# Kernel optimization log

Hardware: AMD Instinct MI355X
Metric: run time of the kernel (lower is better)

## Reference

```python
import jax, jax.numpy as jnp
import numpy as np

B, N, F, H = 1, 8192, 512, 64
NEG_BIAS = -9.0  # GAT adjacency bias for non-edges


def setup_inputs() -> dict:
    key = jax.random.key(0)
    ks = jax.random.split(key, 6)
    features = jax.random.normal(ks[0], (B, N, F), dtype=jnp.float32)
    edge = jax.random.uniform(ks[1], (B, N, N)) < 0.02
    bias_mat = jnp.where(edge, 0.0, NEG_BIAS).astype(jnp.float32)
    W = jax.random.normal(ks[2], (F, H), dtype=jnp.float32) * 0.05   # 1x1 conv, no bias
    a1 = jax.random.normal(ks[3], (H, 1), dtype=jnp.float32) * 0.05  # f_1 1x1 conv
    b1 = jnp.zeros((1,), dtype=jnp.float32)
    a2 = jax.random.normal(ks[4], (H, 1), dtype=jnp.float32) * 0.05  # f_2 1x1 conv
    b2 = jnp.zeros((1,), dtype=jnp.float32)
    return {"features": features, "bias_mat": bias_mat, "W": W,
            "a1": a1, "b1": b1, "a2": a2, "b2": b2}


def reference(features, bias_mat, W, a1, b1, a2, b2):
    # 1x1 conv projection (no bias): [B,N,F] @ [F,H] -> [B,N,H]
    fts = jnp.einsum('bnf,fh->bnh', features, W)
    # per-node scalar attention terms: [B,N,1]
    f1 = jnp.einsum('bnh,ho->bno', fts, a1) + b1
    f2 = jnp.einsum('bnh,ho->bno', fts, a2) + b2
    # additive pairwise logits: [B,N,N]
    logits = f1 + jnp.swapaxes(f2, 1, 2)
    # masked softmax over neighbors, then (as written in source) add bias again
    coefs = jax.nn.softmax(jax.nn.relu(logits) + bias_mat, axis=-1) + bias_mat
    # weighted aggregation: [B,N,N] @ [B,N,H] -> [B,N,H]
    vals = jnp.einsum('bmn,bnh->bmh', coefs, fts)
    return jax.nn.elu(vals)
```

## Files before the change

kernel.cpp:

```cpp
#include <hip/hip_runtime.h>
#include <math.h>

#define N 8192
#define FDIM 512
#define H 64
#define SEG 192

typedef float vf4 __attribute__((ext_vector_type(4)));

__global__ __launch_bounds__(256) void k_fts(const float* __restrict__ feat,
                                             const float* __restrict__ W,
                                             const float* __restrict__ a1v,
                                             const float* __restrict__ b1v,
                                             const float* __restrict__ a2v,
                                             const float* __restrict__ b2v,
                                             float* __restrict__ fts,
                                             float* __restrict__ f1,
                                             float* __restrict__ f2,
                                             float* __restrict__ T) {
    __shared__ float At[64][34];
    __shared__ float Bf[64][64];
    __shared__ float colred[16][64];
    const int t = threadIdx.x;
    const int row0 = blockIdx.x * 32;
    const int hq = (t & 15) * 4;
    const int rq = (t >> 4) * 2;
    float acc[2][4] = {};
    for (int k0 = 0; k0 < FDIM; k0 += 64) {
#pragma unroll
        for (int i = 0; i < 2; ++i) {
            int l = t + i * 256;
            int r = l >> 4;
            int c4 = (l & 15) * 4;
            float4 av = *(const float4*)&feat[(size_t)(row0 + r) * FDIM + k0 + c4];
            At[c4 + 0][r] = av.x; At[c4 + 1][r] = av.y;
            At[c4 + 2][r] = av.z; At[c4 + 3][r] = av.w;
        }
#pragma unroll
        for (int i = 0; i < 4; ++i) {
            int l = t + i * 256;
            int r = l >> 4;
            int c4 = (l & 15) * 4;
            *(float4*)&Bf[r][c4] = *(const float4*)&W[(size_t)(k0 + r) * H + c4];
        }
        __syncthreads();
#pragma unroll 8
        for (int kk = 0; kk < 64; ++kk) {
            float2 a = *(const float2*)&At[kk][rq];
            float4 b = *(const float4*)&Bf[kk][hq];
            acc[0][0] += a.x * b.x; acc[0][1] += a.x * b.y;
            acc[0][2] += a.x * b.z; acc[0][3] += a.x * b.w;
            acc[1][0] += a.y * b.x; acc[1][1] += a.y * b.y;
            acc[1][2] += a.y * b.z; acc[1][3] += a.y * b.w;
        }
        __syncthreads();
    }
#pragma unroll
    for (int j = 0; j < 2; ++j) {
        float4 v = make_float4(acc[j][0], acc[j][1], acc[j][2], acc[j][3]);
        *(float4*)&fts[(size_t)(row0 + rq + j) * H + hq] = v;
    }
    float pa1[4], pa2[4];
#pragma unroll
    for (int i = 0; i < 4; ++i) { pa1[i] = a1v[hq + i]; pa2[i] = a2v[hq + i]; }
#pragma unroll
    for (int j = 0; j < 2; ++j) {
        float s1 = acc[j][0] * pa1[0] + acc[j][1] * pa1[1] + acc[j][2] * pa1[2] + acc[j][3] * pa1[3];
        float s2 = acc[j][0] * pa2[0] + acc[j][1] * pa2[1] + acc[j][2] * pa2[2] + acc[j][3] * pa2[3];
#pragma unroll
        for (int o = 8; o; o >>= 1) { s1 += __shfl_xor(s1, o); s2 += __shfl_xor(s2, o); }
        if ((t & 15) == 0) {
            f1[row0 + rq + j] = s1 + b1v[0];
            f2[row0 + rq + j] = s2 + b2v[0];
        }
    }
#pragma unroll
    for (int i = 0; i < 4; ++i)
        colred[t >> 4][hq + i] = acc[0][i] + acc[1][i];
    __syncthreads();
    if (t < H) {
        float s = 0.f;
#pragma unroll
        for (int g = 0; g < 16; ++g) s += colred[g][t];
        atomicAdd(&T[t], s);
    }
}

__global__ __launch_bounds__(256) void k_all(const float* __restrict__ bias,
                                             const float* __restrict__ fts,
                                             const float* __restrict__ f1g,
                                             const float* __restrict__ f2g,
                                             const float* __restrict__ T,
                                             float* __restrict__ out) {
    __shared__ int    list[4 * SEG];
    __shared__ float2 pairBuf[4 * SEG];
    __shared__ float  redW[4][64];
    __shared__ float  redF[4][64];
    __shared__ float  redE[4];
    const int t = threadIdx.x;
    const int lane = t & 63;
    const int w = t >> 6;
    const int m = blockIdx.x;
    const float f1m = f1g[m];

    const vf4* p = (const vf4*)(bias + (size_t)m * N) + w * 512 + lane;
    vf4 r[8];
#pragma unroll
    for (int j = 0; j < 8; ++j) r[j] = __builtin_nontemporal_load(&p[j * 64]);
    int c = 0;
#pragma unroll
    for (int j = 0; j < 8; ++j)
        c += (r[j].x == 0.f) + (r[j].y == 0.f) + (r[j].z == 0.f) + (r[j].w == 0.f);
    int sc = c;
#pragma unroll
    for (int o = 1; o < 64; o <<= 1) {
        int u = __shfl_up(sc, o);
        if (lane >= o) sc += u;
    }
    const int segBase = w * SEG;
    int pos = segBase + sc - c;
#pragma unroll
    for (int j = 0; j < 8; ++j) {
        int nb = (w * 512 + j * 64 + lane) * 4;
        int m0 = (r[j].x == 0.f), m1 = (r[j].y == 0.f);
        int m2 = (r[j].z == 0.f), m3 = (r[j].w == 0.f);
        if (m0) list[pos] = nb;
        int p1 = pos + m0;
        if (m1) list[p1] = nb + 1;
        int p2 = p1 + m1;
        if (m2) list[p2] = nb + 2;
        int p3 = p2 + m2;
        if (m3) list[p3] = nb + 3;
        pos = p3 + m3;
    }
    int cw = __shfl(sc, 63);
    cw = __builtin_amdgcn_readfirstlane(cw);
    if (cw > SEG) cw = SEG;

    for (int l = lane; l < cw; l += 64) {
        int n = list[segBase + l];
        float ff = f2g[n];
        float ee = __expf(fmaxf(f1m + ff, 0.f));
        pairBuf[segBase + l] = make_float2(ee, __int_as_float(n * 256));
    }

    const char* ftsB = (const char*)fts;
    const int laneOff = lane * 4;
    float accW = 0.f, accF = 0.f, accE = 0.f;
    for (int e = 0; e < cw; e += 8) {
        float2 pr[8];
#pragma unroll
        for (int j = 0; j < 8; ++j) {
            int idx = (e + j < cw) ? (e + j) : (cw - 1);
            pr[j] = pairBuf[segBase + idx];
        }
        float vv[8];
#pragma unroll
        for (int j = 0; j < 8; ++j)
            vv[j] = *(const float*)(ftsB + __float_as_int(pr[j].y) + laneOff);
#pragma unroll
        for (int j = 0; j < 8; ++j) {
            if (e + j < cw) {
                accW += pr[j].x * vv[j];
                accF += vv[j];
                accE += pr[j].x;
            }
        }
    }
    redW[w][lane] = accW;
    redF[w][lane] = accF;
    if (lane == 0) redE[w] = accE;
    __syncthreads();

    if (t < H) {
        float eW = redW[0][t] + redW[1][t] + redW[2][t] + redW[3][t];
        float eF = redF[0][t] + redF[1][t] + redF[2][t] + redF[3][t];
        float eE = redE[0] + redE[1] + redE[2] + redE[3];
        float S = (eE > 0.f) ? eW / eE : 0.f;
        float val = S - 9.0f * (T[t] - eF);
        out[(size_t)m * H + t] = val > 0.f ? val : expm1f(val);
    }
}

extern "C" void kernel_launch(void* const* d_in, const int* in_sizes, int n_in,
                              void* d_out, int out_size, void* d_ws, size_t ws_size,
                              hipStream_t stream) {
    const float* feat = (const float*)d_in[0];
    const float* bias = (const float*)d_in[1];
    const float* W    = (const float*)d_in[2];
    const float* a1   = (const float*)d_in[3];
    const float* b1   = (const float*)d_in[4];
    const float* a2   = (const float*)d_in[5];
    const float* b2   = (const float*)d_in[6];
    float* out = (float*)d_out;

    float* ws  = (float*)d_ws;
    float* fts = ws;
    float* f1  = fts + (size_t)N * H;
    float* f2  = f1 + N;
    float* T   = f2 + N;

    (void)hipMemsetAsync(T, 0, H * sizeof(float), stream);
    hipLaunchKernelGGL(k_fts, dim3(N / 32), dim3(256), 0, stream,
                       feat, W, a1, b1, a2, b2, fts, f1, f2, T);
    hipLaunchKernelGGL(k_all, dim3(N), dim3(256), 0, stream,
                       bias, fts, f1, f2, T, out);
}
```

Before: 390.8 us.

## Use ballot-based compaction, padded edge lists, and smaller projection tiles

Replaces the per-lane count plus shfl_up scan in edge-list compaction with a ballot/mbcnt per element, which removes the scan. The edge list is padded to a multiple of 8 with zero-weight entries that point at a zeroed scratch row, so the gather loop runs without per-element bounds checks and reads pairBuf as float4. The projection kernel now uses 16-row tiles, doubling its block count, and k_all gains an occupancy hint. Costs: more ballots and LDS writes, plus a larger memset to zero the scratch row.

```diff
diff --git a/kernel.cpp b/kernel.cpp
--- a/kernel.cpp
+++ b/kernel.cpp
@@ -5,6 +5,7 @@
 #define FDIM 512
 #define H 64
 #define SEG 192
+#define ZOFF ((N * H + 2 * N + H) * 4)
 
 typedef float vf4 __attribute__((ext_vector_type(4)));
 
@@ -18,65 +19,53 @@
                                              float* __restrict__ f1,
                                              float* __restrict__ f2,
                                              float* __restrict__ T) {
-    __shared__ float At[64][34];
+    __shared__ float At[64][17];
     __shared__ float Bf[64][64];
     __shared__ float colred[16][64];
     const int t = threadIdx.x;
-    const int row0 = blockIdx.x * 32;
+    const int row0 = blockIdx.x * 16;
     const int hq = (t & 15) * 4;
-    const int rq = (t >> 4) * 2;
-    float acc[2][4] = {};
+    const int rq = t >> 4;
+    float acc[4] = {};
     for (int k0 = 0; k0 < FDIM; k0 += 64) {
-#pragma unroll
-        for (int i = 0; i < 2; ++i) {
-            int l = t + i * 256;
-            int r = l >> 4;
-            int c4 = (l & 15) * 4;
+        {
+            const int r = t >> 4;
+            const int c4 = (t & 15) * 4;
             float4 av = *(const float4*)&feat[(size_t)(row0 + r) * FDIM + k0 + c4];
             At[c4 + 0][r] = av.x; At[c4 + 1][r] = av.y;
             At[c4 + 2][r] = av.z; At[c4 + 3][r] = av.w;
         }
 #pragma unroll
         for (int i = 0; i < 4; ++i) {
-            int l = t + i * 256;
-            int r = l >> 4;
-            int c4 = (l & 15) * 4;
-            *(float4*)&Bf[r][c4] = *(const float4*)&W[(size_t)(k0 + r) * H + c4];
+            const int l = t + i * 256;
+            const int rr = l >> 4;
+            const int c4 = (l & 15) * 4;
+            *(float4*)&Bf[rr][c4] = *(const float4*)&W[(size_t)(k0 + rr) * H + c4];
         }
         __syncthreads();
 #pragma unroll 8
         for (int kk = 0; kk < 64; ++kk) {
-            float2 a = *(const float2*)&At[kk][rq];
-            float4 b = *(const float4*)&Bf[kk][hq];
-            acc[0][0] += a.x * b.x; acc[0][1] += a.x * b.y;
-            acc[0][2] += a.x * b.z; acc[0][3] += a.x * b.w;
-            acc[1][0] += a.y * b.x; acc[1][1] += a.y * b.y;
-            acc[1][2] += a.y * b.z; acc[1][3] += a.y * b.w;
+            const float a = At[kk][rq];
+            const float4 b = *(const float4*)&Bf[kk][hq];
+            acc[0] += a * b.x; acc[1] += a * b.y;
+            acc[2] += a * b.z; acc[3] += a * b.w;
         }
         __syncthreads();
     }
-#pragma unroll
-    for (int j = 0; j < 2; ++j) {
-        float4 v = make_float4(acc[j][0], acc[j][1], acc[j][2], acc[j][3]);
-        *(float4*)&fts[(size_t)(row0 + rq + j) * H + hq] = v;
-    }
+    *(float4*)&fts[(size_t)(row0 + rq) * H + hq] = make_float4(acc[0], acc[1], acc[2], acc[3]);
     float pa1[4], pa2[4];
 #pragma unroll
     for (int i = 0; i < 4; ++i) { pa1[i] = a1v[hq + i]; pa2[i] = a2v[hq + i]; }
+    float s1 = acc[0] * pa1[0] + acc[1] * pa1[1] + acc[2] * pa1[2] + acc[3] * pa1[3];
+    float s2 = acc[0] * pa2[0] + acc[1] * pa2[1] + acc[2] * pa2[2] + acc[3] * pa2[3];
 #pragma unroll
-    for (int j = 0; j < 2; ++j) {
-        float s1 = acc[j][0] * pa1[0] + acc[j][1] * pa1[1] + acc[j][2] * pa1[2] + acc[j][3] * pa1[3];
-        float s2 = acc[j][0] * pa2[0] + acc[j][1] * pa2[1] + acc[j][2] * pa2[2] + acc[j][3] * pa2[3];
-#pragma unroll
-        for (int o = 8; o; o >>= 1) { s1 += __shfl_xor(s1, o); s2 += __shfl_xor(s2, o); }
-        if ((t & 15) == 0) {
-            f1[row0 + rq + j] = s1 + b1v[0];
-            f2[row0 + rq + j] = s2 + b2v[0];
-        }
+    for (int o = 8; o; o >>= 1) { s1 += __shfl_xor(s1, o); s2 += __shfl_xor(s2, o); }
+    if ((t & 15) == 0) {
+        f1[row0 + rq] = s1 + b1v[0];
+        f2[row0 + rq] = s2 + b2v[0];
     }
 #pragma unroll
-    for (int i = 0; i < 4; ++i)
-        colred[t >> 4][hq + i] = acc[0][i] + acc[1][i];
+    for (int i = 0; i < 4; ++i) colred[rq][hq + i] = acc[i];
     __syncthreads();
     if (t < H) {
         float s = 0.f;
@@ -86,14 +75,14 @@
     }
 }
 
-__global__ __launch_bounds__(256) void k_all(const float* __restrict__ bias,
-                                             const float* __restrict__ fts,
-                                             const float* __restrict__ f1g,
-                                             const float* __restrict__ f2g,
-                                             const float* __restrict__ T,
-                                             float* __restrict__ out) {
+__global__ __launch_bounds__(256, 4) void k_all(const float* __restrict__ bias,
+                                                const float* __restrict__ fts,
+                                                const float* __restrict__ f1g,
+                                                const float* __restrict__ f2g,
+                                                const float* __restrict__ T,
+                                                float* __restrict__ out) {
     __shared__ int    list[4 * SEG];
-    __shared__ float2 pairBuf[4 * SEG];
+    __shared__ __align__(16) float2 pairBuf[4 * SEG];
     __shared__ float  redW[4][64];
     __shared__ float  redF[4][64];
     __shared__ float  redE[4];
@@ -107,64 +96,57 @@
     vf4 r[8];
 #pragma unroll
     for (int j = 0; j < 8; ++j) r[j] = __builtin_nontemporal_load(&p[j * 64]);
-    int c = 0;
-#pragma unroll
-    for (int j = 0; j < 8; ++j)
-        c += (r[j].x == 0.f) + (r[j].y == 0.f) + (r[j].z == 0.f) + (r[j].w == 0.f);
-    int sc = c;
-#pragma unroll
-    for (int o = 1; o < 64; o <<= 1) {
-        int u = __shfl_up(sc, o);
-        if (lane >= o) sc += u;
-    }
+
     const int segBase = w * SEG;
-    int pos = segBase + sc - c;
+    int base = segBase;
 #pragma unroll
     for (int j = 0; j < 8; ++j) {
-        int nb = (w * 512 + j * 64 + lane) * 4;
-        int m0 = (r[j].x == 0.f), m1 = (r[j].y == 0.f);
-        int m2 = (r[j].z == 0.f), m3 = (r[j].w == 0.f);
-        if (m0) list[pos] = nb;
-        int p1 = pos + m0;
-        if (m1) list[p1] = nb + 1;
-        int p2 = p1 + m1;
-        if (m2) list[p2] = nb + 2;
-        int p3 = p2 + m2;
-        if (m3) list[p3] = nb + 3;
-        pos = p3 + m3;
+        const int nb = (w * 512 + j * 64 + lane) * 4;
+#pragma unroll
+        for (int k = 0; k < 4; ++k) {
+            const float v = (k == 0) ? r[j].x : (k == 1) ? r[j].y : (k == 2) ? r[j].z : r[j].w;
+            const bool e = (v == 0.f);
+            const unsigned long long mk = __ballot(e);
+            const int below = __builtin_amdgcn_mbcnt_hi((unsigned)(mk >> 32),
+                              __builtin_amdgcn_mbcnt_lo((unsigned)mk, 0));
+            if (e) list[base + below] = nb + k;
+            base += (int)__popcll(mk);
+        }
     }
-    int cw = __shfl(sc, 63);
-    cw = __builtin_amdgcn_readfirstlane(cw);
+    int cw = base - segBase;
     if (cw > SEG) cw = SEG;
+    const int cwPad = (cw + 7) & ~7;
 
-    for (int l = lane; l < cw; l += 64) {
-        int n = list[segBase + l];
-        float ff = f2g[n];
-        float ee = __expf(fmaxf(f1m + ff, 0.f));
-        pairBuf[segBase + l] = make_float2(ee, __int_as_float(n * 256));
+    for (int l = lane; l < cwPad; l += 64) {
+        float2 pr;
+        if (l < cw) {
+            const int n = list[segBase + l];
+            pr = make_float2(__expf(fmaxf(f1m + f2g[n], 0.f)), __int_as_float(n * 256));
+        } else {
+            pr = make_float2(0.f, __int_as_float(ZOFF));
+        }
+        pairBuf[segBase + l] = pr;
     }
 
     const char* ftsB = (const char*)fts;
     const int laneOff = lane * 4;
+    const float4* pb4 = (const float4*)pairBuf;
     float accW = 0.f, accF = 0.f, accE = 0.f;
-    for (int e = 0; e < cw; e += 8) {
-        float2 pr[8];
+    for (int e = 0; e < cwPad; e += 8) {
+        float4 q[4];
 #pragma unroll
-        for (int j = 0; j < 8; ++j) {
-            int idx = (e + j < cw) ? (e + j) : (cw - 1);
-            pr[j] = pairBuf[segBase + idx];
-        }
+        for (int j = 0; j < 4; ++j) q[j] = pb4[(segBase + e) / 2 + j];
         float vv[8];
 #pragma unroll
-        for (int j = 0; j < 8; ++j)
-            vv[j] = *(const float*)(ftsB + __float_as_int(pr[j].y) + laneOff);
+        for (int j = 0; j < 4; ++j) {
+            vv[2 * j]     = *(const float*)(ftsB + __float_as_int(q[j].y) + laneOff);
+            vv[2 * j + 1] = *(const float*)(ftsB + __float_as_int(q[j].w) + laneOff);
+        }
 #pragma unroll
-        for (int j = 0; j < 8; ++j) {
-            if (e + j < cw) {
-                accW += pr[j].x * vv[j];
-                accF += vv[j];
-                accE += pr[j].x;
-            }
+        for (int j = 0; j < 4; ++j) {
+            accW += q[j].x * vv[2 * j] + q[j].z * vv[2 * j + 1];
+            accF += vv[2 * j] + vv[2 * j + 1];
+            accE += q[j].x + q[j].z;
         }
     }
     redW[w][lane] = accW;
@@ -200,8 +182,8 @@
     float* f2  = f1 + N;
     float* T   = f2 + N;
 
-    (void)hipMemsetAsync(T, 0, H * sizeof(float), stream);
-    hipLaunchKernelGGL(k_fts, dim3(N / 32), dim3(256), 0, stream,
+    (void)hipMemsetAsync(T, 0, (H + 64) * sizeof(float), stream);
+    hipLaunchKernelGGL(k_fts, dim3(N / 16), dim3(256), 0, stream,
                        feat, W, a1, b1, a2, b2, fts, f1, f2, T);
     hipLaunchKernelGGL(k_all, dim3(N), dim3(256), 0, stream,
                        bias, fts, f1, f2, T, out);
```

Result: no change. 392.7 us (+0.5%).
